# Kernel tuning notes

Measured on AMD Instinct MI355X. Metric: run time of the kernel, lower is better.

Reference implementation:

```python
import jax, jax.numpy as jnp
import numpy as np

N_NODES = 100_000
N_EDGES = 1_600_000
D_IN = 128
D_HID = 128
D_OUT = 128
N_GRAPHS = 1024


def setup_inputs() -> dict:
    key = jax.random.key(0)
    ks = jax.random.split(key, 7)
    x = jax.random.normal(ks[0], (N_NODES, D_IN), dtype=jnp.float32)
    edge_index = jax.random.randint(ks[1], (2, N_EDGES), 0, N_NODES, dtype=jnp.int32)
    batch = jnp.sort(jax.random.randint(ks[2], (N_NODES,), 0, N_GRAPHS, dtype=jnp.int32))
    W1 = jax.random.normal(ks[3], (D_IN, D_HID), dtype=jnp.float32) * (1.0 / np.sqrt(D_IN))
    b1 = jax.random.normal(ks[4], (D_HID,), dtype=jnp.float32) * 0.01
    W2 = jax.random.normal(ks[5], (D_HID, D_OUT), dtype=jnp.float32) * (1.0 / np.sqrt(D_HID))
    b2 = jax.random.normal(ks[6], (D_OUT,), dtype=jnp.float32) * 0.01
    return {"x": x, "edge_index": edge_index, "batch": batch,
            "W1": W1, "b1": b1, "W2": W2, "b2": b2, "num_graphs": N_GRAPHS}


def gcn_conv(x, edge_index, W, b):
    """PyG GCNConv: add self-loops, symmetric deg^{-1/2} norm, linear, scatter-add."""
    n = x.shape[0]
    xw = x @ W  # [N, H] -- transform before propagate, as PyG does
    loop = jnp.arange(n, dtype=edge_index.dtype)
    src = jnp.concatenate([edge_index[0], loop])  # message source (x_j)
    dst = jnp.concatenate([edge_index[1], loop])  # aggregation target
    deg = jax.ops.segment_sum(jnp.ones_like(dst, dtype=xw.dtype), dst, num_segments=n)
    dinv = jnp.where(deg > 0, jax.lax.rsqrt(deg), 0.0)
    norm = dinv[src] * dinv[dst]  # [E+N]
    out = jax.ops.segment_sum(norm[:, None] * xw[src], dst, num_segments=n)
    return out + b


def reference(x, edge_index, batch, W1, b1, W2, b2, num_graphs):
    h = jax.nn.relu(gcn_conv(x, edge_index, W1, b1))
    h = gcn_conv(h, edge_index, W2, b2)
    # global_mean_pool over graph ids
    s = jax.ops.segment_sum(h, batch, num_segments=num_graphs)          # [G, D_OUT]
    cnt = jax.ops.segment_sum(jnp.ones((x.shape[0],), h.dtype), batch, num_segments=num_graphs)
    return s / jnp.maximum(cnt, 1.0)[:, None]
```

## Files before the change

### kernel.cpp

```cpp
#include <hip/hip_runtime.h>

constexpr int D = 128;
constexpr int PAD = 48;
constexpr int EBLK = 4096;
constexpr int WNODE = 256;
constexpr int CAPW = 32;
constexpr int SCAP = 8192;

typedef __attribute__((ext_vector_type(8))) short short8;
typedef __attribute__((ext_vector_type(4))) float floatx4;
typedef __attribute__((ext_vector_type(2))) float floatx2;
typedef unsigned short ushort_t;
typedef unsigned char uchar_t;

static inline size_t ws_align(size_t x) { return (x + 255) & ~size_t(255); }

__device__ inline unsigned pack_bf16(float a, float b) {
  unsigned ua = __float_as_uint(a), ub = __float_as_uint(b);
  ua += 0x7fffu + ((ua >> 16) & 1u);
  ub += 0x7fffu + ((ub >> 16) & 1u);
  return ((ua >> 16) & 0xffffu) | (ub & 0xffff0000u);
}
__device__ inline ushort_t f32_to_bf16u(float f) {
  unsigned u = __float_as_uint(f);
  u += 0x7fffu + ((u >> 16) & 1u);
  return (ushort_t)(u >> 16);
}
__device__ inline float bf16u_to_f32(ushort_t u) {
  return __uint_as_float(((unsigned)u) << 16);
}
__device__ inline uchar_t f32_to_fp8(float v) {
  int p = __builtin_amdgcn_cvt_pk_fp8_f32(v, v, 0, false);
  return (uchar_t)(p & 0xff);
}
__device__ inline void fp8x4_acc(unsigned u, float* v) {
  floatx2 a = __builtin_amdgcn_cvt_pk_f32_fp8((int)u, false);
  floatx2 b = __builtin_amdgcn_cvt_pk_f32_fp8((int)u, true);
  v[0] += a.x; v[1] += a.y; v[2] += b.x; v[3] += b.y;
}
__device__ inline void fp8x4_acc2(unsigned u, floatx2* v) {
  v[0] += __builtin_amdgcn_cvt_pk_f32_fp8((int)u, false);
  v[1] += __builtin_amdgcn_cvt_pk_f32_fp8((int)u, true);
}

__global__ __launch_bounds__(256) void k_prep(
    const int* __restrict__ src, const int* __restrict__ dst, int E,
    int nstrips, int nw,
    unsigned* __restrict__ bucket, int* __restrict__ bkcnt,
    uint2* __restrict__ spill, int* __restrict__ scnt,
    const float* __restrict__ W1, const float* __restrict__ W2,
    ushort_t* __restrict__ w1t, ushort_t* __restrict__ w2t, int nbin) {
  const int b = blockIdx.x;
  const int t = threadIdx.x;
  if (b < nbin) {
    __shared__ int lcnt[512];
    for (int i = t; i < nw; i += 256) lcnt[i] = 0;
    __syncthreads();
    const int base = b * EBLK;
    const int end = min(base + EBLK, E);
    for (int j = base + t; j < end; j += 256) {
      int ss = src[j], dd = dst[j];
      int wnd = dd >> 8;
      unsigned pk = ((unsigned)(dd & 255) << 17) | (unsigned)ss;
      int p = atomicAdd(&lcnt[wnd], 1);
      if (p < CAPW) {
        bucket[((size_t)wnd * nstrips + b) * CAPW + p] = pk;
      } else {
        int sp = atomicAdd(scnt, 1);
        if (sp < SCAP) spill[sp] = make_uint2((unsigned)ss, (unsigned)dd);
      }
    }
    __syncthreads();
    for (int i = t; i < nw; i += 256)
      bkcnt[(size_t)i * nstrips + b] = min(lcnt[i], CAPW);
    return;
  }
  {
    int idx = (b - nbin) * 256 + t;
    int k = idx >> 7, n = idx & 127;
    w1t[n * 128 + k] = f32_to_bf16u(W1[idx]);
    w2t[n * 128 + k] = f32_to_bf16u(W2[idx]);
  }
}

__global__ __launch_bounds__(256) void k_fill(
    const unsigned* __restrict__ bucket, const int* __restrict__ bkcnt,
    const uint2* __restrict__ spill, const int* __restrict__ scnt,
    int* __restrict__ cnt, int* __restrict__ csrp, int N, int nstrips) {
  __shared__ int lc[WNODE];
  __shared__ int ls[WNODE * PAD];
  const int w = blockIdx.x;
  const int t = threadIdx.x;
  const int wbase = w << 8;
  const int nn = min(WNODE, N - wbase);
  for (int i = t; i < WNODE; i += 256) lc[i] = 0;
  __syncthreads();
  const int* bc = bkcnt + (size_t)w * nstrips;
  const unsigned* bwin = bucket + (size_t)w * nstrips * CAPW;
  const int wid = t >> 6, l = t & 63;
  const int sgrp = l >> 3;
  const int ui = l & 7;
  for (int sb0 = wid * 8; sb0 < nstrips; sb0 += 32) {
    int s = sb0 + sgrp;
    int c = (s < nstrips) ? bc[s] : 0;
    uint4 v = make_uint4(0u, 0u, 0u, 0u);
    if (ui * 4 < c)
      v = ((const uint4*)(bwin + (size_t)s * CAPW))[ui];
    unsigned e[4] = {v.x, v.y, v.z, v.w};
#pragma unroll
    for (int u = 0; u < 4; ++u) {
      int j = ui * 4 + u;
      if (j < c) {
        unsigned pk = e[u];
        int dl = (int)(pk >> 17);
        int p = atomicAdd(&lc[dl], 1);
        if (p < PAD) ls[dl * PAD + p] = (int)(pk & 0x1FFFFu);
      }
    }
  }
  {
    int ns = min(*scnt, SCAP);
    for (int j = t; j < ns; j += 256) {
      uint2 e = spill[j];
      if ((int)(e.y >> 8) == w) {
        int dl = (int)(e.y & 255u);
        int p = atomicAdd(&lc[dl], 1);
        if (p < PAD) ls[dl * PAD + p] = (int)e.x;
      }
    }
  }
  __syncthreads();
  const int total = nn * PAD;
  int4* dp = (int4*)(csrp + (size_t)wbase * PAD);
  const int4* sp = (const int4*)ls;
  for (int i = t; i < (total >> 2); i += 256) dp[i] = sp[i];
  for (int i = (total & ~3) + t; i < total; i += 256)
    csrp[(size_t)wbase * PAD + i] = ls[i];
  for (int i = t; i < nn; i += 256) cnt[wbase + i] = lc[i];
}

template <bool A_FP32>
__global__ __launch_bounds__(512) void k_gemm(
    const void* __restrict__ Av, const ushort_t* __restrict__ Wt,
    const int* __restrict__ cnt, uchar_t* __restrict__ Y, int N) {
  __shared__ ushort_t As[128 * 128];
  __shared__ ushort_t Bs[128 * 128];
  const int t = threadIdx.x;
  const int rowBase = blockIdx.x * 128;

  {
    const uint4* g = (const uint4*)Wt;
#pragma unroll
    for (int i = 0; i < 4; ++i) {
      int idx = t + 512 * i;
      int r = idx >> 4, c = idx & 15;
      int cs = c ^ (r & 15);
      *(uint4*)&Bs[r * 128 + cs * 8] = g[idx];
    }
  }
  if (A_FP32) {
    const float4* A = (const float4*)Av;
#pragma unroll
    for (int i = 0; i < 8; ++i) {
      int idx = t + 512 * i;
      int r = idx >> 5, c4 = idx & 31;
      int grow = rowBase + r;
      float4 v = make_float4(0.f, 0.f, 0.f, 0.f);
      if (grow < N) v = A[(size_t)grow * 32 + c4];
      int cs = (c4 >> 1) ^ (r & 15);
      unsigned* p = (unsigned*)&As[r * 128 + cs * 8 + (c4 & 1) * 4];
      p[0] = pack_bf16(v.x, v.y);
      p[1] = pack_bf16(v.z, v.w);
    }
  } else {
    const uint4* A = (const uint4*)Av;
#pragma unroll
    for (int i = 0; i < 4; ++i) {
      int idx = t + 512 * i;
      int r = idx >> 4, c = idx & 15;
      int grow = rowBase + r;
      uint4 v = make_uint4(0u, 0u, 0u, 0u);
      if (grow < N) v = A[(size_t)grow * 16 + c];
      int cs = c ^ (r & 15);
      *(uint4*)&As[r * 128 + cs * 8] = v;
    }
  }
  __syncthreads();

  const int w = t >> 6;
  const int l = t & 63;
  const int qd = l >> 4, lm = l & 15;
  const int mrow = w * 16;

  floatx4 acc[8];
#pragma unroll
  for (int j = 0; j < 8; ++j) acc[j] = (floatx4){0.f, 0.f, 0.f, 0.f};

#pragma unroll
  for (int ks = 0; ks < 4; ++ks) {
    const int ch = ks * 4 + qd;
    const int chs = ch ^ lm;
    short8 a0 = *(const short8*)&As[(mrow + lm) * 128 + chs * 8];
#pragma unroll
    for (int j = 0; j < 8; ++j) {
      short8 b = *(const short8*)&Bs[(j * 16 + lm) * 128 + chs * 8];
      acc[j] = __builtin_amdgcn_mfma_f32_16x16x32_bf16(a0, b, acc[j], 0, 0, 0);
    }
  }

  float s[4];
#pragma unroll
  for (int r = 0; r < 4; ++r) {
    int grow = rowBase + mrow + qd * 4 + r;
    s[r] = (grow < N) ? rsqrtf(1.f + (float)cnt[grow]) : 0.f;
  }
#pragma unroll
  for (int j = 0; j < 8; ++j)
#pragma unroll
    for (int r = 0; r < 4; ++r) {
      int grow = rowBase + mrow + qd * 4 + r;
      if (grow < N)
        Y[(size_t)grow * 128 + j * 16 + lm] = f32_to_fp8(s[r] * acc[j][r]);
    }
}

template <bool RELU>
__global__ __launch_bounds__(256) void k_aggregate(
    const uchar_t* __restrict__ y, const int* __restrict__ csrp,
    const int* __restrict__ cnt, const float* __restrict__ bias,
    ushort_t* __restrict__ out, int N) {
  const int wid = threadIdx.x >> 6;
  const int n0 = blockIdx.x * 8 + wid * 2;
  if (n0 >= N) return;
  const int n1 = n0 + 1;
  const bool hasB = (n1 < N);
  const int l = threadIdx.x & 63;
  const int eg = l >> 4, q = l & 15;
  const uint2* yb = (const uint2*)y;
  int degA0 = cnt[n0];
  int degB0 = hasB ? cnt[n1] : 0;
  float dvA = rsqrtf(1.f + (float)degA0);
  float dvB = rsqrtf(1.f + (float)degB0);
  int degA = degA0 > PAD ? PAD : degA0;
  int degB = degB0 > PAD ? PAD : degB0;
  int idxA = 0, idxB = 0;
  if (l < PAD) {
    idxA = csrp[(size_t)n0 * PAD + l];
    if (hasB) idxB = csrp[(size_t)n1 * PAD + l];
  }
  uint2 sv = make_uint2(0u, 0u);
  if (eg == 0) sv = yb[(size_t)n0 * 16 + q];
  else if (eg == 1 && hasB) sv = yb[(size_t)n1 * 16 + q];
  floatx2 vA[4], vB[4];
#pragma unroll
  for (int k = 0; k < 4; ++k) { vA[k] = (floatx2){0.f, 0.f}; vB[k] = (floatx2){0.f, 0.f}; }
  const int dmax = degA > degB ? degA : degB;
  const int iters = (dmax + 15) >> 4;
  for (int it = 0; it < iters; ++it) {
    int p0 = it * 16 + eg;
    int p1 = p0 + 4, p2 = p0 + 8, p3 = p0 + 12;
    int a0 = __shfl(idxA, p0);
    int a1 = __shfl(idxA, p1);
    int a2 = __shfl(idxA, p2);
    int a3 = __shfl(idxA, p3);
    int b0 = __shfl(idxB, p0);
    int b1 = __shfl(idxB, p1);
    int b2 = __shfl(idxB, p2);
    int b3 = __shfl(idxB, p3);
    if (p0 < degA) { uint2 v = yb[(size_t)a0 * 16 + q]; fp8x4_acc2(v.x, vA); fp8x4_acc2(v.y, vA + 2); }
    if (p0 < degB) { uint2 v = yb[(size_t)b0 * 16 + q]; fp8x4_acc2(v.x, vB); fp8x4_acc2(v.y, vB + 2); }
    if (p1 < degA) { uint2 v = yb[(size_t)a1 * 16 + q]; fp8x4_acc2(v.x, vA); fp8x4_acc2(v.y, vA + 2); }
    if (p1 < degB) { uint2 v = yb[(size_t)b1 * 16 + q]; fp8x4_acc2(v.x, vB); fp8x4_acc2(v.y, vB + 2); }
    if (p2 < degA) { uint2 v = yb[(size_t)a2 * 16 + q]; fp8x4_acc2(v.x, vA); fp8x4_acc2(v.y, vA + 2); }
    if (p2 < degB) { uint2 v = yb[(size_t)b2 * 16 + q]; fp8x4_acc2(v.x, vB); fp8x4_acc2(v.y, vB + 2); }
    if (p3 < degA) { uint2 v = yb[(size_t)a3 * 16 + q]; fp8x4_acc2(v.x, vA); fp8x4_acc2(v.y, vA + 2); }
    if (p3 < degB) { uint2 v = yb[(size_t)b3 * 16 + q]; fp8x4_acc2(v.x, vB); fp8x4_acc2(v.y, vB + 2); }
  }
  float fA[8] = {vA[0].x, vA[0].y, vA[1].x, vA[1].y, vA[2].x, vA[2].y, vA[3].x, vA[3].y};
  float fB[8] = {vB[0].x, vB[0].y, vB[1].x, vB[1].y, vB[2].x, vB[2].y, vB[3].x, vB[3].y};
#pragma unroll
  for (int k = 0; k < 8; ++k) {
    fA[k] += __shfl_xor(fA[k], 32); fA[k] += __shfl_xor(fA[k], 16);
    fB[k] += __shfl_xor(fB[k], 32); fB[k] += __shfl_xor(fB[k], 16);
  }
  if (eg == 0 || (eg == 1 && hasB)) {
    float dv = (eg == 0) ? dvA : dvB;
    int node = (eg == 0) ? n0 : n1;
    float f[8];
#pragma unroll
    for (int k = 0; k < 8; ++k) f[k] = (eg == 0) ? fA[k] : fB[k];
    fp8x4_acc(sv.x, f); fp8x4_acc(sv.y, f + 4);
    float4 c0 = ((const float4*)bias)[2 * q];
    float4 c1 = ((const float4*)bias)[2 * q + 1];
    float o[8];
    o[0] = dv * f[0] + c0.x; o[1] = dv * f[1] + c0.y;
    o[2] = dv * f[2] + c0.z; o[3] = dv * f[3] + c0.w;
    o[4] = dv * f[4] + c1.x; o[5] = dv * f[5] + c1.y;
    o[6] = dv * f[6] + c1.z; o[7] = dv * f[7] + c1.w;
    if (RELU) {
#pragma unroll
      for (int k = 0; k < 8; ++k) o[k] = fmaxf(o[k], 0.f);
    }
    uint4 pk;
    pk.x = pack_bf16(o[0], o[1]); pk.y = pack_bf16(o[2], o[3]);
    pk.z = pack_bf16(o[4], o[5]); pk.w = pack_bf16(o[6], o[7]);
    ((uint4*)out)[(size_t)node * 16 + q] = pk;
  }
}

__global__ __launch_bounds__(512) void k_pool(
    const ushort_t* __restrict__ h, const int* __restrict__ batch,
    float* __restrict__ out, int N, int G) {
  __shared__ float part[4][128];
  int g = blockIdx.x;
  int col = threadIdx.x & 127;
  int pr = threadIdx.x >> 7;
  int lo = 0, hi = N;
  while (lo < hi) { int m = (lo + hi) >> 1; if (batch[m] < g) lo = m + 1; else hi = m; }
  int start = lo;
  hi = N;
  while (lo < hi) { int m = (lo + hi) >> 1; if (batch[m] <= g) lo = m + 1; else hi = m; }
  int end = lo;
  float sum = 0.f;
  for (int r = start + pr; r < end; r += 4) sum += bf16u_to_f32(h[(size_t)r * D + col]);
  part[pr][col] = sum;
  __syncthreads();
  if (pr == 0) {
    float s = part[0][col] + part[1][col] + part[2][col] + part[3][col];
    int c = end - start;
    out[(size_t)g * D + col] = s / (float)(c > 0 ? c : 1);
  }
}

extern "C" void kernel_launch(void* const* d_in, const int* in_sizes, int n_in,
                              void* d_out, int out_size, void* d_ws, size_t ws_size,
                              hipStream_t stream) {
  const float* x  = (const float*)d_in[0];
  const int* edge = (const int*)d_in[1];
  const int* batch = (const int*)d_in[2];
  const float* W1 = (const float*)d_in[3];
  const float* b1 = (const float*)d_in[4];
  const float* W2 = (const float*)d_in[5];
  const float* b2 = (const float*)d_in[6];
  float* out = (float*)d_out;

  const int N = in_sizes[0] / D;
  const int E = in_sizes[1] / 2;
  const int G = out_size / D;
  const int* esrc = edge;
  const int* edst = edge + E;

  const int nstrips = (E + EBLK - 1) / EBLK;
  const int nw = (N + WNODE - 1) / WNODE;

  char* ws = (char*)d_ws;
  size_t off = 0;
  auto alloc = [&](size_t bytes) {
    char* p = ws + off;
    off = ws_align(off + bytes);
    return p;
  };
  uchar_t* bufY = (uchar_t*)alloc((size_t)N * D);
  ushort_t* bufH = (ushort_t*)alloc((size_t)N * D * 2);
  int* cnt = (int*)alloc((size_t)N * 4);
  int* csrp = (int*)alloc((size_t)N * PAD * 4);
  ushort_t* w1t = (ushort_t*)alloc((size_t)D * D * 2);
  ushort_t* w2t = (ushort_t*)alloc((size_t)D * D * 2);
  unsigned* bucket = (unsigned*)alloc((size_t)nw * nstrips * CAPW * 4);
  int* bkcnt = (int*)alloc((size_t)nw * nstrips * 4);
  uint2* spill = (uint2*)alloc((size_t)SCAP * 8);
  int* scnt = (int*)alloc(256);

  const int tb = 256;

  hipMemsetAsync(scnt, 0, 4, stream);

  const int nbin = nstrips;
  const int nwp = (D * D) / 256;
  k_prep<<<nbin + nwp, tb, 0, stream>>>(esrc, edst, E, nstrips, nw,
                                        bucket, bkcnt, spill, scnt,
                                        W1, W2, w1t, w2t, nbin);

  k_fill<<<nw, tb, 0, stream>>>(bucket, bkcnt, spill, scnt, cnt, csrp, N, nstrips);

  const int gblk = (N + 127) / 128;
  const int ablk = (N + 7) / 8;
  k_gemm<true><<<gblk, 512, 0, stream>>>(x, w1t, cnt, bufY, N);
  k_aggregate<true><<<ablk, 256, 0, stream>>>(bufY, csrp, cnt, b1, bufH, N);
  k_gemm<false><<<gblk, 512, 0, stream>>>(bufH, w2t, cnt, bufY, N);
  k_aggregate<false><<<ablk, 256, 0, stream>>>(bufY, csrp, cnt, b2, bufH, N);
  k_pool<<<G, 512, 0, stream>>>(bufH, batch, out, N, G);
}
```

Before: 265.4 us.

## Halve GEMM row tile and aggregate four nodes per wavefront

The GEMM now processes 64 rows per block, with each pair of waves splitting the 128 output columns, so there are twice as many blocks and less LDS per block. The aggregate kernel now handles four nodes per wavefront instead of two, so all four 16-lane groups issue gathers, their loop trip count set by the largest of the four degrees. The goal is more memory-level parallelism in the gather-bound aggregation and better occupancy in the GEMM. The cost is that the weight tile is reloaded by more GEMM blocks, the aggregate uses more registers, and divergence grows because the loop runs to the maximum degree of four nodes.

```diff
diff --git a/kernel.cpp b/kernel.cpp
--- a/kernel.cpp
+++ b/kernel.cpp
@@ -143,10 +143,10 @@
 __global__ __launch_bounds__(512) void k_gemm(
     const void* __restrict__ Av, const ushort_t* __restrict__ Wt,
     const int* __restrict__ cnt, uchar_t* __restrict__ Y, int N) {
-  __shared__ ushort_t As[128 * 128];
+  __shared__ ushort_t As[64 * 128];
   __shared__ ushort_t Bs[128 * 128];
   const int t = threadIdx.x;
-  const int rowBase = blockIdx.x * 128;
+  const int rowBase = blockIdx.x * 64;
 
   {
     const uint4* g = (const uint4*)Wt;
@@ -161,7 +161,7 @@
   if (A_FP32) {
     const float4* A = (const float4*)Av;
 #pragma unroll
-    for (int i = 0; i < 8; ++i) {
+    for (int i = 0; i < 4; ++i) {
       int idx = t + 512 * i;
       int r = idx >> 5, c4 = idx & 31;
       int grow = rowBase + r;
@@ -175,7 +175,7 @@
   } else {
     const uint4* A = (const uint4*)Av;
 #pragma unroll
-    for (int i = 0; i < 4; ++i) {
+    for (int i = 0; i < 2; ++i) {
       int idx = t + 512 * i;
       int r = idx >> 4, c = idx & 15;
       int grow = rowBase + r;
@@ -190,11 +190,12 @@
   const int w = t >> 6;
   const int l = t & 63;
   const int qd = l >> 4, lm = l & 15;
-  const int mrow = w * 16;
-
-  floatx4 acc[8];
-#pragma unroll
-  for (int j = 0; j < 8; ++j) acc[j] = (floatx4){0.f, 0.f, 0.f, 0.f};
+  const int mrow = (w >> 1) * 16;
+  const int jb = (w & 1) * 4;
+
+  floatx4 acc[4];
+#pragma unroll
+  for (int j = 0; j < 4; ++j) acc[j] = (floatx4){0.f, 0.f, 0.f, 0.f};
 
 #pragma unroll
   for (int ks = 0; ks < 4; ++ks) {
@@ -202,8 +203,8 @@
     const int chs = ch ^ lm;
     short8 a0 = *(const short8*)&As[(mrow + lm) * 128 + chs * 8];
 #pragma unroll
-    for (int j = 0; j < 8; ++j) {
-      short8 b = *(const short8*)&Bs[(j * 16 + lm) * 128 + chs * 8];
+    for (int j = 0; j < 4; ++j) {
+      short8 b = *(const short8*)&Bs[((jb + j) * 16 + lm) * 128 + chs * 8];
       acc[j] = __builtin_amdgcn_mfma_f32_16x16x32_bf16(a0, b, acc[j], 0, 0, 0);
     }
   }
@@ -215,12 +216,12 @@
     s[r] = (grow < N) ? rsqrtf(1.f + (float)cnt[grow]) : 0.f;
   }
 #pragma unroll
-  for (int j = 0; j < 8; ++j)
+  for (int j = 0; j < 4; ++j)
 #pragma unroll
     for (int r = 0; r < 4; ++r) {
       int grow = rowBase + mrow + qd * 4 + r;
       if (grow < N)
-        Y[(size_t)grow * 128 + j * 16 + lm] = f32_to_fp8(s[r] * acc[j][r]);
+        Y[(size_t)grow * 128 + (jb + j) * 16 + lm] = f32_to_fp8(s[r] * acc[j][r]);
     }
 }
 
@@ -230,65 +231,71 @@
     const int* __restrict__ cnt, const float* __restrict__ bias,
     ushort_t* __restrict__ out, int N) {
   const int wid = threadIdx.x >> 6;
-  const int n0 = blockIdx.x * 8 + wid * 2;
-  if (n0 >= N) return;
-  const int n1 = n0 + 1;
-  const bool hasB = (n1 < N);
+  const int base = blockIdx.x * 16 + wid * 4;
+  if (base >= N) return;
   const int l = threadIdx.x & 63;
   const int eg = l >> 4, q = l & 15;
   const uint2* yb = (const uint2*)y;
-  int degA0 = cnt[n0];
-  int degB0 = hasB ? cnt[n1] : 0;
-  float dvA = rsqrtf(1.f + (float)degA0);
-  float dvB = rsqrtf(1.f + (float)degB0);
-  int degA = degA0 > PAD ? PAD : degA0;
-  int degB = degB0 > PAD ? PAD : degB0;
-  int idxA = 0, idxB = 0;
-  if (l < PAD) {
-    idxA = csrp[(size_t)n0 * PAD + l];
-    if (hasB) idxB = csrp[(size_t)n1 * PAD + l];
+  int degc[4], idx[4];
+  float dvv[4];
+#pragma unroll
+  for (int k = 0; k < 4; ++k) {
+    int n = base + k;
+    bool has = (n < N);
+    int d0 = has ? cnt[n] : 0;
+    dvv[k] = rsqrtf(1.f + (float)d0);
+    degc[k] = d0 > PAD ? PAD : d0;
+    idx[k] = 0;
+    if (l < PAD && has) idx[k] = csrp[(size_t)n * PAD + l];
   }
   uint2 sv = make_uint2(0u, 0u);
-  if (eg == 0) sv = yb[(size_t)n0 * 16 + q];
-  else if (eg == 1 && hasB) sv = yb[(size_t)n1 * 16 + q];
-  floatx2 vA[4], vB[4];
-#pragma unroll
-  for (int k = 0; k < 4; ++k) { vA[k] = (floatx2){0.f, 0.f}; vB[k] = (floatx2){0.f, 0.f}; }
-  const int dmax = degA > degB ? degA : degB;
+  {
+    int nself = base + eg;
+    if (nself < N) sv = yb[(size_t)nself * 16 + q];
+  }
+  floatx2 v[4][4];
+#pragma unroll
+  for (int k = 0; k < 4; ++k)
+#pragma unroll
+    for (int j = 0; j < 4; ++j) v[k][j] = (floatx2){0.f, 0.f};
+  int dmax = degc[0];
+#pragma unroll
+  for (int k = 1; k < 4; ++k) dmax = degc[k] > dmax ? degc[k] : dmax;
   const int iters = (dmax + 15) >> 4;
   for (int it = 0; it < iters; ++it) {
     int p0 = it * 16 + eg;
     int p1 = p0 + 4, p2 = p0 + 8, p3 = p0 + 12;
-    int a0 = __shfl(idxA, p0);
-    int a1 = __shfl(idxA, p1);
-    int a2 = __shfl(idxA, p2);
-    int a3 = __shfl(idxA, p3);
-    int b0 = __shfl(idxB, p0);
-    int b1 = __shfl(idxB, p1);
-    int b2 = __shfl(idxB, p2);
-    int b3 = __shfl(idxB, p3);
-    if (p0 < degA) { uint2 v = yb[(size_t)a0 * 16 + q]; fp8x4_acc2(v.x, vA); fp8x4_acc2(v.y, vA + 2); }
-    if (p0 < degB) { uint2 v = yb[(size_t)b0 * 16 + q]; fp8x4_acc2(v.x, vB); fp8x4_acc2(v.y, vB + 2); }
-    if (p1 < degA) { uint2 v = yb[(size_t)a1 * 16 + q]; fp8x4_acc2(v.x, vA); fp8x4_acc2(v.y, vA + 2); }
-    if (p1 < degB) { uint2 v = yb[(size_t)b1 * 16 + q]; fp8x4_acc2(v.x, vB); fp8x4_acc2(v.y, vB + 2); }
-    if (p2 < degA) { uint2 v = yb[(size_t)a2 * 16 + q]; fp8x4_acc2(v.x, vA); fp8x4_acc2(v.y, vA + 2); }
-    if (p2 < degB) { uint2 v = yb[(size_t)b2 * 16 + q]; fp8x4_acc2(v.x, vB); fp8x4_acc2(v.y, vB + 2); }
-    if (p3 < degA) { uint2 v = yb[(size_t)a3 * 16 + q]; fp8x4_acc2(v.x, vA); fp8x4_acc2(v.y, vA + 2); }
-    if (p3 < degB) { uint2 v = yb[(size_t)b3 * 16 + q]; fp8x4_acc2(v.x, vB); fp8x4_acc2(v.y, vB + 2); }
-  }
-  float fA[8] = {vA[0].x, vA[0].y, vA[1].x, vA[1].y, vA[2].x, vA[2].y, vA[3].x, vA[3].y};
-  float fB[8] = {vB[0].x, vB[0].y, vB[1].x, vB[1].y, vB[2].x, vB[2].y, vB[3].x, vB[3].y};
-#pragma unroll
-  for (int k = 0; k < 8; ++k) {
-    fA[k] += __shfl_xor(fA[k], 32); fA[k] += __shfl_xor(fA[k], 16);
-    fB[k] += __shfl_xor(fB[k], 32); fB[k] += __shfl_xor(fB[k], 16);
-  }
-  if (eg == 0 || (eg == 1 && hasB)) {
-    float dv = (eg == 0) ? dvA : dvB;
-    int node = (eg == 0) ? n0 : n1;
-    float f[8];
-#pragma unroll
-    for (int k = 0; k < 8; ++k) f[k] = (eg == 0) ? fA[k] : fB[k];
+#pragma unroll
+    for (int k = 0; k < 4; ++k) {
+      int s0 = __shfl(idx[k], p0);
+      int s1 = __shfl(idx[k], p1);
+      int s2 = __shfl(idx[k], p2);
+      int s3 = __shfl(idx[k], p3);
+      if (p0 < degc[k]) { uint2 t2 = yb[(size_t)s0 * 16 + q]; fp8x4_acc2(t2.x, v[k]); fp8x4_acc2(t2.y, v[k] + 2); }
+      if (p1 < degc[k]) { uint2 t2 = yb[(size_t)s1 * 16 + q]; fp8x4_acc2(t2.x, v[k]); fp8x4_acc2(t2.y, v[k] + 2); }
+      if (p2 < degc[k]) { uint2 t2 = yb[(size_t)s2 * 16 + q]; fp8x4_acc2(t2.x, v[k]); fp8x4_acc2(t2.y, v[k] + 2); }
+      if (p3 < degc[k]) { uint2 t2 = yb[(size_t)s3 * 16 + q]; fp8x4_acc2(t2.x, v[k]); fp8x4_acc2(t2.y, v[k] + 2); }
+    }
+  }
+  float f[8];
+  float dv = 0.f;
+#pragma unroll
+  for (int k = 0; k < 4; ++k) {
+    float tt[8] = {v[k][0].x, v[k][0].y, v[k][1].x, v[k][1].y,
+                   v[k][2].x, v[k][2].y, v[k][3].x, v[k][3].y};
+#pragma unroll
+    for (int j = 0; j < 8; ++j) {
+      tt[j] += __shfl_xor(tt[j], 32);
+      tt[j] += __shfl_xor(tt[j], 16);
+    }
+    if (eg == k) {
+#pragma unroll
+      for (int j = 0; j < 8; ++j) f[j] = tt[j];
+      dv = dvv[k];
+    }
+  }
+  const int node = base + eg;
+  if (node < N) {
     fp8x4_acc(sv.x, f); fp8x4_acc(sv.y, f + 4);
     float4 c0 = ((const float4*)bias)[2 * q];
     float4 c1 = ((const float4*)bias)[2 * q + 1];
@@ -383,8 +390,8 @@
 
   k_fill<<<nw, tb, 0, stream>>>(bucket, bkcnt, spill, scnt, cnt, csrp, N, nstrips);
 
-  const int gblk = (N + 127) / 128;
-  const int ablk = (N + 7) / 8;
+  const int gblk = (N + 63) / 64;
+  const int ablk = (N + 15) / 16;
   k_gemm<true><<<gblk, 512, 0, stream>>>(x, w1t, cnt, bufY, N);
   k_aggregate<true><<<ablk, 256, 0, stream>>>(bufY, csrp, cnt, b1, bufH, N);
   k_gemm<false><<<gblk, 512, 0, stream>>>(bufH, w2t, cnt, bufY, N);
```

After: 283.2 us. 6.7% more time.
